# Kernel tuning notes

Measured on AMD Instinct MI355X. Metric: run time of the kernel, lower is better.

## Reference

```python
import jax, jax.numpy as jnp
import numpy as np

NPROTOS = 40      # forced by init_offset_tensor reshape
NCLASS  = 512     # number of child classes
C       = 64      # genetic feature channels (pshape[0])
W       = 40      # genetic sequence width (hard-coded in offset tensor)
B       = 1024    # batch
P       = NPROTOS * NCLASS  # 20480 total prototypes
EPS     = 1e-12   # F.normalize eps


def _build_last_layer_weight():
    # match[j, j // nprotos] = 1, weight = match.T with zeros -> -0.5
    match = np.zeros((P, NCLASS), np.float32)
    match[np.arange(P), np.arange(P) // NPROTOS] = 1.0
    w = match.T.copy()
    w[w == 0] = -0.5
    return jnp.asarray(w)


def _build_offset_tensor():
    # arange2[i, j] = (i - j) % nprotos; nprotos == 40 so arange3 is empty
    i = np.arange(NPROTOS)[:, None]
    j = np.arange(NPROTOS)[None, :]
    ar2 = (i - j) % NPROTOS                                  # (40, 40)
    off = np.tile(ar2.reshape(NPROTOS, 1, 1, NPROTOS), (NCLASS, C, 1, 1))
    return jnp.asarray(off.astype(np.int32))                 # (P, C, 1, W)


def setup_inputs() -> dict:
    key = jax.random.key(0)
    k1, k2 = jax.random.split(key)
    conv_features = jax.random.normal(k1, (B, C, 1, W), dtype=jnp.float32)
    prototype = jax.random.uniform(k2, (P, C, 1, 1), dtype=jnp.float32)  # torch.rand
    return {
        "conv_features": conv_features,
        "prototype": prototype,
        "last_layer_weight": _build_last_layer_weight(),
        "offset_tensor": _build_offset_tensor(),
    }


def _l2norm(x, axis):
    # F.normalize: x / max(||x||_2, eps)
    return x / jnp.maximum(jnp.linalg.norm(x, axis=axis, keepdims=True), EPS)


def reference(conv_features, prototype, last_layer_weight, offset_tensor):
    sqrt_D = 1.0  # sqrt(pshape[1] * pshape[2]) = sqrt(1*1)
    x = _l2norm(conv_features, axis=1) / sqrt_D              # (B, C, 1, W)
    p = _l2norm(prototype, axis=1) / sqrt_D                  # (P, C, 1, 1)
    # pad prototypes to width W, then per-prototype spatial offset gather
    p = jnp.pad(p, ((0, 0), (0, 0), (0, 0), (0, W - 1)))     # (P, C, 1, W)
    p = jnp.take_along_axis(p, offset_tensor, axis=3)        # (P, C, 1, W)
    # conv2d with full-width kernel -> output (B, P, 1, 1); max_pool over 1x1 is identity
    sim = jnp.einsum('bchw,pchw->bp', x, p)                  # (B, P)
    min_distances = -sim                                     # view(-1, nclass*nprotos)
    logits = sim @ last_layer_weight.T                       # (B, NCLASS)
    return (logits, min_distances)
```

## Files before the change

kernel.cpp:

```cpp
#include <hip/hip_runtime.h>
#include <hip/hip_fp16.h>
#include <math.h>

#define NB 1024
#define NC 64
#define NW 40
#define NK 512
#define NP 20480
#define EPSF 1e-12f


__global__ __launch_bounds__(256) void knorm(const float* __restrict__ conv,
                                             const float* __restrict__ proto,
                                             __half* __restrict__ xnh,
                                             __half* __restrict__ pnh) {
    __shared__ float xs[64 * 41];
    __shared__ float rn[40];
    int blk = blockIdx.x;
    if (blk < NB) {
        int b = blk;
        const float* xb = conv + b * (64 * 40);
        for (int t = threadIdx.x; t < 2560; t += 256) {
            int c = t / 40, w = t % 40;
            xs[c * 41 + w] = xb[t];
        }
        __syncthreads();
        if (threadIdx.x < 40) {
            int w = threadIdx.x;
            float s = 0.f;
#pragma unroll
            for (int c = 0; c < 64; ++c) { float v = xs[c * 41 + w]; s += v * v; }
            rn[w] = 1.0f / fmaxf(sqrtf(s), EPSF);
        }
        __syncthreads();
        for (int t = threadIdx.x; t < 2560; t += 256) {
            int w = t >> 6, c = t & 63;
            xnh[((size_t)w * NB + b) * 64 + c] = __float2half(xs[c * 41 + w] * rn[w]);
        }
    } else {
        int p = (blk - NB) * 4 + (threadIdx.x >> 6);
        int lane = threadIdx.x & 63;
        float v = proto[p * 64 + lane];
        float s = v * v;
#pragma unroll
        for (int off = 32; off >= 1; off >>= 1) s += __shfl_xor(s, off);
        float r = 1.0f / fmaxf(sqrtf(s), EPSF);
        int j = p % NW, k = p / NW;
        pnh[((size_t)j * NK + k) * 64 + lane] = __float2half(v * r);
    }
}

__global__ __launch_bounds__(256, 2) void kgemm(const __half* __restrict__ xnh,
                                                const __half* __restrict__ pnh,
                                                __half* __restrict__ simt) {
    __shared__ float4 Xs[128 * 16];
    __shared__ float4 Ps[128 * 16];
    int b0 = blockIdx.x * 128;
    int k0 = blockIdx.y * 128;
    int j  = blockIdx.z;
    const __half* xg = xnh + ((size_t)j * NB + b0) * 64;
    const __half* pg = pnh + ((size_t)j * NK + k0) * 64;

    for (int g = threadIdx.x; g < 1024; g += 256) {
        int row = g >> 3, ch = g & 7;
        uint4 ux = *(const uint4*)(xg + (size_t)row * 64 + ch * 8);
        uint4 up = *(const uint4*)(pg + (size_t)row * 64 + ch * 8);
        float2 x01 = __half22float2(*(__half2*)&ux.x);
        float2 x23 = __half22float2(*(__half2*)&ux.y);
        float2 x45 = __half22float2(*(__half2*)&ux.z);
        float2 x67 = __half22float2(*(__half2*)&ux.w);
        float2 p01 = __half22float2(*(__half2*)&up.x);
        float2 p23 = __half22float2(*(__half2*)&up.y);
        float2 p45 = __half22float2(*(__half2*)&up.z);
        float2 p67 = __half22float2(*(__half2*)&up.w);
        int xk = row & 7, pk = (row >> 3) & 7;
        int c4a = ch * 2, c4b = ch * 2 + 1;
        Xs[(row << 4) + (c4a ^ xk)] = make_float4(x01.x, x01.y, x23.x, x23.y);
        Xs[(row << 4) + (c4b ^ xk)] = make_float4(x45.x, x45.y, x67.x, x67.y);
        Ps[(row << 4) + (c4a ^ pk)] = make_float4(p01.x, p01.y, p23.x, p23.y);
        Ps[(row << 4) + (c4b ^ pk)] = make_float4(p45.x, p45.y, p67.x, p67.y);
    }
    __syncthreads();

    int tb = threadIdx.x >> 4, tk = threadIdx.x & 15;
    float acc[8][8];
#pragma unroll
    for (int i = 0; i < 8; ++i)
#pragma unroll
        for (int q = 0; q < 8; ++q) acc[i][q] = 0.f;

    for (int c4 = 0; c4 < 16; ++c4) {
        float4 xv[8];
#pragma unroll
        for (int i = 0; i < 8; ++i) {
            int row = tb + 16 * i;
            xv[i] = Xs[(row << 4) + (c4 ^ (row & 7))];
        }
#pragma unroll
        for (int q = 0; q < 8; ++q) {
            int row = tk * 8 + q;
            float4 pv = Ps[(row << 4) + (c4 ^ (tk & 7))];
#pragma unroll
            for (int i = 0; i < 8; ++i)
                acc[i][q] += xv[i].x * pv.x + xv[i].y * pv.y +
                             xv[i].z * pv.z + xv[i].w * pv.w;
        }
    }

#pragma unroll
    for (int i = 0; i < 8; ++i) {
        int b = b0 + tb + 16 * i;
        union { __half2 h2[4]; uint4 u; } st;
        st.h2[0] = __halves2half2(__float2half(acc[i][0]), __float2half(acc[i][1]));
        st.h2[1] = __halves2half2(__float2half(acc[i][2]), __float2half(acc[i][3]));
        st.h2[2] = __halves2half2(__float2half(acc[i][4]), __float2half(acc[i][5]));
        st.h2[3] = __halves2half2(__float2half(acc[i][6]), __float2half(acc[i][7]));
        *(uint4*)(simt + (size_t)b * NP + j * NK + k0 + tk * 8) = st.u;
    }
}

__global__ __launch_bounds__(256) void ktrans(const __half* __restrict__ simt,
                                              float* __restrict__ out) {
    __shared__ __half ldh[40][520];
    __shared__ float wred[4];
    int b = blockIdx.x;
    int t = threadIdx.x;
    const __half* src = simt + (size_t)b * NP;
    float* md = out + (size_t)NB * NK + (size_t)b * NP;
    float rk[2];
    float my_tot = 0.f;

#pragma unroll
    for (int kp = 0; kp < 2; ++kp) {
        int k0 = kp << 8;
#pragma unroll
        for (int r = 0; r < 5; ++r) {
            int idx = r * 256 + t;
            int j = idx >> 5, ch = idx & 31;
            uint4 v = *(const uint4*)(src + j * NK + k0 + ch * 8);
            *(uint4*)(&ldh[j][ch * 8]) = v;
        }
        __syncthreads();
        {
            float s = 0.f;
#pragma unroll
            for (int j = 0; j < 40; ++j) s += __half2float(ldh[j][t]);
            rk[kp] = s;
            my_tot += s;
        }
#pragma unroll
        for (int r = 0; r < 10; ++r) {
            int pl = (r * 256 + t) * 4;
            int kk = pl / 40, jj = pl - kk * 40;
            float w[4];
#pragma unroll
            for (int e = 0; e < 4; ++e) {
                w[e] = -__half2float(ldh[jj][kk]);
                if (++jj == 40) { jj = 0; ++kk; }
            }
            *(float4*)(md + k0 * 40 + pl) = make_float4(w[0], w[1], w[2], w[3]);
        }
        __syncthreads();
    }

    float s = my_tot;
#pragma unroll
    for (int off = 32; off >= 1; off >>= 1) s += __shfl_xor(s, off);
    if ((t & 63) == 0) wred[t >> 6] = s;
    __syncthreads();
    float S = wred[0] + wred[1] + wred[2] + wred[3];
    out[(size_t)b * NK + t]       = 1.5f * rk[0] - 0.5f * S;
    out[(size_t)b * NK + 256 + t] = 1.5f * rk[1] - 0.5f * S;
}

extern "C" void kernel_launch(void* const* d_in, const int* in_sizes, int n_in,
                              void* d_out, int out_size, void* d_ws, size_t ws_size,
                              hipStream_t stream) {
    (void)in_sizes; (void)n_in; (void)out_size; (void)ws_size;
    const float* conv  = (const float*)d_in[0];
    const float* proto = (const float*)d_in[1];
    float* out = (float*)d_out;
    char* wsb = (char*)d_ws;
    __half* xnh  = (__half*)(wsb);
    __half* pnh  = (__half*)(wsb + 5242880);
    __half* simt = (__half*)(wsb + 7864320);

    knorm<<<6144, 256, 0, stream>>>(conv, proto, xnh, pnh);
    kgemm<<<dim3(8, 4, 40), 256, 0, stream>>>(xnh, pnh, simt);
    ktrans<<<1024, 256, 0, stream>>>(simt, out);
}
```

Before: 339.8 us.

## Fuse GEMM with transpose using MFMA and drop the fp16 sim intermediate

Replaces the FP32 FMA LDS-tiled GEMM with MFMA 16x16x32 f16 instructions that read operands straight from global memory. The transpose into min_distances and the per-class sums move into the same kernel through an LDS staging buffer and LDS atomics, so the 40 MB fp16 sim matrix is never written and reread. A small kernel then forms the logits from the per-class sums. The trade-offs are small 16x32 tiles with no operand reuse through LDS, and a smaller reduction kernel that still has to run afterwards.

```diff
diff --git a/kernel.cpp b/kernel.cpp
--- a/kernel.cpp
+++ b/kernel.cpp
@@ -8,6 +8,9 @@
 #define NK 512
 #define NP 20480
 #define EPSF 1e-12f
+
+typedef _Float16 f16x8 __attribute__((ext_vector_type(8)));
+typedef float f32x4 __attribute__((ext_vector_type(4)));
 
 
 __global__ __launch_bounds__(256) void knorm(const float* __restrict__ conv,
@@ -50,127 +53,89 @@
     }
 }
 
-__global__ __launch_bounds__(256, 2) void kgemm(const __half* __restrict__ xnh,
-                                                const __half* __restrict__ pnh,
-                                                __half* __restrict__ simt) {
-    __shared__ float4 Xs[128 * 16];
-    __shared__ float4 Ps[128 * 16];
-    int b0 = blockIdx.x * 128;
-    int k0 = blockIdx.y * 128;
-    int j  = blockIdx.z;
-    const __half* xg = xnh + ((size_t)j * NB + b0) * 64;
-    const __half* pg = pnh + ((size_t)j * NK + k0) * 64;
+__global__ __launch_bounds__(256) void kfused(const __half* __restrict__ xnh,
+                                              const __half* __restrict__ pnh,
+                                              float* __restrict__ sk_out,
+                                              float* __restrict__ out) {
+    __shared__ __half mds[16 * 32 * 44];
+    __shared__ float sks[16][32];
+    int t = threadIdx.x;
+    int w = t >> 6, l = t & 63;
+    int row = l & 15, g = l >> 4;
+    int b0 = blockIdx.x * 16;
+    int k0 = blockIdx.y * 32;
 
-    for (int g = threadIdx.x; g < 1024; g += 256) {
-        int row = g >> 3, ch = g & 7;
-        uint4 ux = *(const uint4*)(xg + (size_t)row * 64 + ch * 8);
-        uint4 up = *(const uint4*)(pg + (size_t)row * 64 + ch * 8);
-        float2 x01 = __half22float2(*(__half2*)&ux.x);
-        float2 x23 = __half22float2(*(__half2*)&ux.y);
-        float2 x45 = __half22float2(*(__half2*)&ux.z);
-        float2 x67 = __half22float2(*(__half2*)&ux.w);
-        float2 p01 = __half22float2(*(__half2*)&up.x);
-        float2 p23 = __half22float2(*(__half2*)&up.y);
-        float2 p45 = __half22float2(*(__half2*)&up.z);
-        float2 p67 = __half22float2(*(__half2*)&up.w);
-        int xk = row & 7, pk = (row >> 3) & 7;
-        int c4a = ch * 2, c4b = ch * 2 + 1;
-        Xs[(row << 4) + (c4a ^ xk)] = make_float4(x01.x, x01.y, x23.x, x23.y);
-        Xs[(row << 4) + (c4b ^ xk)] = make_float4(x45.x, x45.y, x67.x, x67.y);
-        Ps[(row << 4) + (c4a ^ pk)] = make_float4(p01.x, p01.y, p23.x, p23.y);
-        Ps[(row << 4) + (c4b ^ pk)] = make_float4(p45.x, p45.y, p67.x, p67.y);
-    }
+    for (int i = t; i < 512; i += 256) sks[i >> 5][i & 31] = 0.f;
     __syncthreads();
 
-    int tb = threadIdx.x >> 4, tk = threadIdx.x & 15;
-    float acc[8][8];
+    const __half* xbase = xnh + ((size_t)b0 + row) * 64 + g * 8;
+    const __half* pbase = pnh + ((size_t)k0 + row) * 64 + g * 8;
+    float skacc[2][4] = {{0.f, 0.f, 0.f, 0.f}, {0.f, 0.f, 0.f, 0.f}};
+
 #pragma unroll
-    for (int i = 0; i < 8; ++i)
+    for (int jj = 0; jj < 10; ++jj) {
+        int j = w * 10 + jj;
+        const __half* xj = xbase + (size_t)j * (NB * 64);
+        const __half* pj = pbase + (size_t)j * (NK * 64);
+        f16x8 a0 = *(const f16x8*)(xj);
+        f16x8 a1 = *(const f16x8*)(xj + 32);
 #pragma unroll
-        for (int q = 0; q < 8; ++q) acc[i][q] = 0.f;
-
-    for (int c4 = 0; c4 < 16; ++c4) {
-        float4 xv[8];
+        for (int f = 0; f < 2; ++f) {
+            f16x8 q0 = *(const f16x8*)(pj + (size_t)f * 16 * 64);
+            f16x8 q1 = *(const f16x8*)(pj + (size_t)f * 16 * 64 + 32);
+            f32x4 acc = {0.f, 0.f, 0.f, 0.f};
+            acc = __builtin_amdgcn_mfma_f32_16x16x32_f16(a0, q0, acc, 0, 0, 0);
+            acc = __builtin_amdgcn_mfma_f32_16x16x32_f16(a1, q1, acc, 0, 0, 0);
+            int kl = f * 16 + row;
 #pragma unroll
-        for (int i = 0; i < 8; ++i) {
-            int row = tb + 16 * i;
-            xv[i] = Xs[(row << 4) + (c4 ^ (row & 7))];
-        }
-#pragma unroll
-        for (int q = 0; q < 8; ++q) {
-            int row = tk * 8 + q;
-            float4 pv = Ps[(row << 4) + (c4 ^ (tk & 7))];
-#pragma unroll
-            for (int i = 0; i < 8; ++i)
-                acc[i][q] += xv[i].x * pv.x + xv[i].y * pv.y +
-                             xv[i].z * pv.z + xv[i].w * pv.w;
+            for (int r = 0; r < 4; ++r) {
+                int bl = g * 4 + r;
+                skacc[f][r] += acc[r];
+                mds[(bl * 32 + kl) * 44 + j] = __float2half(acc[r]);
+            }
         }
     }
+#pragma unroll
+    for (int f = 0; f < 2; ++f)
+#pragma unroll
+        for (int r = 0; r < 4; ++r)
+            atomicAdd(&sks[g * 4 + r][f * 16 + row], skacc[f][r]);
+    __syncthreads();
 
+    for (int i = t; i < 512; i += 256) {
+        int b = i >> 5, k = i & 31;
+        sk_out[((size_t)b0 + b) * NK + k0 + k] = sks[b][k];
+    }
+    float* md = out + (size_t)NB * NK;
 #pragma unroll
-    for (int i = 0; i < 8; ++i) {
-        int b = b0 + tb + 16 * i;
-        union { __half2 h2[4]; uint4 u; } st;
-        st.h2[0] = __halves2half2(__float2half(acc[i][0]), __float2half(acc[i][1]));
-        st.h2[1] = __halves2half2(__float2half(acc[i][2]), __float2half(acc[i][3]));
-        st.h2[2] = __halves2half2(__float2half(acc[i][4]), __float2half(acc[i][5]));
-        st.h2[3] = __halves2half2(__float2half(acc[i][6]), __float2half(acc[i][7]));
-        *(uint4*)(simt + (size_t)b * NP + j * NK + k0 + tk * 8) = st.u;
+    for (int i = 0; i < 20; ++i) {
+        int gi = i * 256 + t;
+        int b = gi / 320;
+        int r = gi - b * 320;
+        int k = r / 10;
+        int j0 = (r - k * 10) * 4;
+        uint2 u = *(const uint2*)(mds + (b * 32 + k) * 44 + j0);
+        float2 v01 = __half22float2(*(__half2*)&u.x);
+        float2 v23 = __half22float2(*(__half2*)&u.y);
+        *(float4*)(md + ((size_t)b0 + b) * NP + ((size_t)k0 + k) * 40 + j0) =
+            make_float4(-v01.x, -v01.y, -v23.x, -v23.y);
     }
 }
 
-__global__ __launch_bounds__(256) void ktrans(const __half* __restrict__ simt,
-                                              float* __restrict__ out) {
-    __shared__ __half ldh[40][520];
-    __shared__ float wred[4];
-    int b = blockIdx.x;
-    int t = threadIdx.x;
-    const __half* src = simt + (size_t)b * NP;
-    float* md = out + (size_t)NB * NK + (size_t)b * NP;
-    float rk[2];
-    float my_tot = 0.f;
-
-#pragma unroll
-    for (int kp = 0; kp < 2; ++kp) {
-        int k0 = kp << 8;
-#pragma unroll
-        for (int r = 0; r < 5; ++r) {
-            int idx = r * 256 + t;
-            int j = idx >> 5, ch = idx & 31;
-            uint4 v = *(const uint4*)(src + j * NK + k0 + ch * 8);
-            *(uint4*)(&ldh[j][ch * 8]) = v;
-        }
-        __syncthreads();
-        {
-            float s = 0.f;
-#pragma unroll
-            for (int j = 0; j < 40; ++j) s += __half2float(ldh[j][t]);
-            rk[kp] = s;
-            my_tot += s;
-        }
-#pragma unroll
-        for (int r = 0; r < 10; ++r) {
-            int pl = (r * 256 + t) * 4;
-            int kk = pl / 40, jj = pl - kk * 40;
-            float w[4];
-#pragma unroll
-            for (int e = 0; e < 4; ++e) {
-                w[e] = -__half2float(ldh[jj][kk]);
-                if (++jj == 40) { jj = 0; ++kk; }
-            }
-            *(float4*)(md + k0 * 40 + pl) = make_float4(w[0], w[1], w[2], w[3]);
-        }
-        __syncthreads();
-    }
-
-    float s = my_tot;
+__global__ __launch_bounds__(256) void klogits(const float* __restrict__ sk,
+                                               float* __restrict__ out) {
+    __shared__ float w4[4];
+    int b = blockIdx.x, t = threadIdx.x;
+    float a = sk[(size_t)b * NK + t];
+    float c = sk[(size_t)b * NK + 256 + t];
+    float s = a + c;
 #pragma unroll
     for (int off = 32; off >= 1; off >>= 1) s += __shfl_xor(s, off);
-    if ((t & 63) == 0) wred[t >> 6] = s;
+    if ((t & 63) == 0) w4[t >> 6] = s;
     __syncthreads();
-    float S = wred[0] + wred[1] + wred[2] + wred[3];
-    out[(size_t)b * NK + t]       = 1.5f * rk[0] - 0.5f * S;
-    out[(size_t)b * NK + 256 + t] = 1.5f * rk[1] - 0.5f * S;
+    float tot = w4[0] + w4[1] + w4[2] + w4[3];
+    out[(size_t)b * NK + t]       = 1.5f * a - 0.5f * tot;
+    out[(size_t)b * NK + 256 + t] = 1.5f * c - 0.5f * tot;
 }
 
 extern "C" void kernel_launch(void* const* d_in, const int* in_sizes, int n_in,
@@ -181,11 +146,11 @@
     const float* proto = (const float*)d_in[1];
     float* out = (float*)d_out;
     char* wsb = (char*)d_ws;
-    __half* xnh  = (__half*)(wsb);
-    __half* pnh  = (__half*)(wsb + 5242880);
-    __half* simt = (__half*)(wsb + 7864320);
+    __half* xnh = (__half*)(wsb);
+    __half* pnh = (__half*)(wsb + 5242880);
+    float*  sk  = (float*)(wsb + 7864320);
 
     knorm<<<6144, 256, 0, stream>>>(conv, proto, xnh, pnh);
-    kgemm<<<dim3(8, 4, 40), 256, 0, stream>>>(xnh, pnh, simt);
-    ktrans<<<1024, 256, 0, stream>>>(simt, out);
+    kfused<<<dim3(64, 16), 256, 0, stream>>>(xnh, pnh, sk, out);
+    klogits<<<1024, 256, 0, stream>>>(sk, out);
 }
```

After: 316.7 us. 6.8% less time.
